# Performance work log

Hardware: AMD Instinct MI355X
Metric: run time of the kernel (lower is better)

## Reference

```python
import jax, jax.numpy as jnp
import numpy as np

NEG_INF = -9e15
NEG_SLOPE = 0.2

def setup_inputs() -> dict:
    key = jax.random.key(0)
    k1, k2, k3, k4 = jax.random.split(key, 4)
    N, d_in, d_out = 8192, 256, 256
    x = jax.random.normal(k1, (N, d_in), dtype=jnp.float32)
    adj = jax.random.randint(k2, (N, N), 0, 2).astype(jnp.float32)
    W = jax.random.normal(k3, (d_in, d_out), dtype=jnp.float32) * (1.0 / np.sqrt(d_in))
    a = jax.random.normal(k4, (2 * d_out,), dtype=jnp.float32) * (1.0 / np.sqrt(2 * d_out))
    return {"x": x, "adj": adj, "W": W, "a": a}

def reference(x, adj, W, a):
    d_out = W.shape[1]
    Wh = x @ W                                   # [N, d_out]
    # a([Wh_i || Wh_j]) decomposed: e_ij = <a_src, Wh_i> + <a_dst, Wh_j>
    e_src = Wh @ a[:d_out]                       # [N]
    e_dst = Wh @ a[d_out:]                       # [N]
    e = jax.nn.leaky_relu(e_src[:, None] + e_dst[None, :], NEG_SLOPE)  # [N, N]
    N = Wh.shape[0]
    mask = (adj > 0) | jnp.eye(N, dtype=bool)
    e = jnp.where(mask, e, NEG_INF)
    alpha = jax.nn.softmax(e, axis=1)            # [N, N]
    h = alpha @ Wh                               # [N, d_out]
    return h
```

## Files before the change

kernel.cpp:

```cpp
#include <hip/hip_runtime.h>
#include <stdint.h>

#define N 8192
#define D 256

typedef __attribute__((ext_vector_type(4))) float f32x4;
typedef __attribute__((ext_vector_type(8))) short bf16x8;

__device__ __forceinline__ unsigned short f2bf(float f) {
    unsigned u = __float_as_uint(f);
    u += 0x7fff + ((u >> 16) & 1);
    return (unsigned short)(u >> 16);
}
__device__ __forceinline__ float leaky(float x) {
    return fmaxf(x, 0.f) + 0.2f * fminf(x, 0.f);
}
__device__ __forceinline__ void sync_lds() {
    asm volatile("s_waitcnt lgkmcnt(0)\n\ts_barrier" ::: "memory");
}

__global__ __launch_bounds__(256) void k0_compress(const float* __restrict__ adj,
                                                   unsigned int* __restrict__ mask) {
    const int idx = blockIdx.x * 256 + threadIdx.x;
    const int r = idx >> 8;
    const int ww = idx & 255;
    const float* src = adj + ((size_t)idx << 5);
    unsigned int bits = 0;
#pragma unroll
    for (int j = 0; j < 8; ++j) {
        float4 v = *(const float4*)(src + j * 4);
        bits |= (v.x > 0.f ? 1u : 0u) << (j * 4 + 0);
        bits |= (v.y > 0.f ? 1u : 0u) << (j * 4 + 1);
        bits |= (v.z > 0.f ? 1u : 0u) << (j * 4 + 2);
        bits |= (v.w > 0.f ? 1u : 0u) << (j * 4 + 3);
    }
    if ((r >> 5) == ww) bits |= 1u << (r & 31);
    mask[idx] = bits;
}

#define K1_BM 16
__global__ __launch_bounds__(256) void k1_gemm(const float* __restrict__ x,
                                               const float* __restrict__ W,
                                               float* __restrict__ Wh,
                                               unsigned short* __restrict__ WhT) {
    __shared__ float xsT[32][20];
    const int t = threadIdx.x;
    const int r0 = blockIdx.x * K1_BM;
    float acc[K1_BM];
#pragma unroll
    for (int i = 0; i < K1_BM; ++i) acc[i] = 0.f;

    for (int k0 = 0; k0 < D; k0 += 32) {
        __syncthreads();
        if (t < 128) {
            int r = t >> 3, ks = (t & 7) * 4;
            float4 v = *(const float4*)(x + (size_t)(r0 + r) * D + k0 + ks);
            xsT[ks + 0][r] = v.x; xsT[ks + 1][r] = v.y;
            xsT[ks + 2][r] = v.z; xsT[ks + 3][r] = v.w;
        }
        __syncthreads();
#pragma unroll 8
        for (int kk = 0; kk < 32; ++kk) {
            float wv = W[(size_t)(k0 + kk) * D + t];
#pragma unroll
            for (int rc = 0; rc < K1_BM / 4; ++rc) {
                float4 xv = *(const float4*)&xsT[kk][rc * 4];
                acc[rc * 4 + 0] += xv.x * wv;
                acc[rc * 4 + 1] += xv.y * wv;
                acc[rc * 4 + 2] += xv.z * wv;
                acc[rc * 4 + 3] += xv.w * wv;
            }
        }
    }
#pragma unroll
    for (int r = 0; r < K1_BM; ++r) Wh[(size_t)(r0 + r) * D + t] = acc[r];
    unsigned short pk[K1_BM];
#pragma unroll
    for (int r = 0; r < K1_BM; ++r) pk[r] = f2bf(acc[r]);
    uint4* dst = (uint4*)(WhT + (size_t)t * N + r0);
    dst[0] = *(uint4*)&pk[0];
    dst[1] = *(uint4*)&pk[8];
}

__global__ __launch_bounds__(256) void k2_edot(const float* __restrict__ Wh,
                                               const float* __restrict__ a,
                                               float* __restrict__ e_src,
                                               float* __restrict__ e_dst) {
    const int wave = threadIdx.x >> 6, lane = threadIdx.x & 63;
    const int row = blockIdx.x * 4 + wave;
    float4 wv = *(const float4*)(Wh + (size_t)row * D + lane * 4);
    float4 as = *(const float4*)(a + lane * 4);
    float4 ad = *(const float4*)(a + D + lane * 4);
    float ps = wv.x * as.x + wv.y * as.y + wv.z * as.z + wv.w * as.w;
    float pd = wv.x * ad.x + wv.y * ad.y + wv.z * ad.z + wv.w * ad.w;
#pragma unroll
    for (int m = 1; m < 64; m <<= 1) {
        ps += __shfl_xor(ps, m);
        pd += __shfl_xor(pd, m);
    }
    if (lane == 0) { e_src[row] = ps; e_dst[row] = pd; }
}

__global__ __launch_bounds__(256) void k3_max(const float* __restrict__ e_dst,
                                              float* __restrict__ maxdst) {
    __shared__ float red[4];
    const int t = threadIdx.x;
    float m = -3.4e38f;
    for (int i = t; i < N; i += 256) m = fmaxf(m, e_dst[i]);
#pragma unroll
    for (int msk = 1; msk < 64; msk <<= 1) m = fmaxf(m, __shfl_xor(m, msk));
    if ((t & 63) == 0) red[t >> 6] = m;
    __syncthreads();
    if (t == 0) *maxdst = fmaxf(fmaxf(red[0], red[1]), fmaxf(red[2], red[3]));
}

#define BM 64
#define BK 64
#define RB (N / BM)
#define SPLITS 8
#define NITER ((N / SPLITS) / BK)
#define PSTRIDE 72
__global__ __launch_bounds__(512, 4) void k4_main(const unsigned char* __restrict__ mask,
                                                  const unsigned short* __restrict__ WhT,
                                                  const float* __restrict__ e_src,
                                                  const float* __restrict__ e_dst,
                                                  const float* __restrict__ maxdst,
                                                  float* __restrict__ O_part,
                                                  float* __restrict__ l_part) {
    __shared__ unsigned short p_lds[2][BM][PSTRIDE];

    const int t = threadIdx.x;
    const int rb = blockIdx.x & (RB - 1);
    const int s  = blockIdx.x >> 7;
    const int r0 = rb * BM;
    const int j0 = s * (N / SPLITS);

    const int pr = t >> 3;
    const int pcw = t & 7;
    const int pc = pcw * 8;
    const int gr = r0 + pr;

    const int w = t >> 6;
    const int lane = t & 63;
    const int quad = lane >> 4, lo = lane & 15;

    const float md = *maxdst;
    const float es = e_src[gr];
    const float m = leaky(es + md);

    f32x4 acc[4][2];
#pragma unroll
    for (int mt = 0; mt < 4; ++mt)
#pragma unroll
        for (int nt = 0; nt < 2; ++nt)
            acc[mt][nt] = (f32x4){0.f, 0.f, 0.f, 0.f};
    float lsum = 0.f;

    const unsigned char* mrow = mask + (size_t)gr * (N / 8) + (j0 >> 3) + pcw;
    const float* ed_row = e_dst + j0 + pc;
    const unsigned short* wt_base = WhT + (size_t)(w * 32 + lo) * N + j0 + quad * 8;

    unsigned int mb;
    float4 edv0, edv1;
    bf16x8 bfr[2][2];

    mb = mrow[0];
    edv0 = *(const float4*)(ed_row);
    edv1 = *(const float4*)(ed_row + 4);
#pragma unroll
    for (int ks2 = 0; ks2 < 2; ++ks2)
#pragma unroll
        for (int nt = 0; nt < 2; ++nt)
            bfr[ks2][nt] = *(const bf16x8*)(wt_base + (size_t)nt * (16 * N) + ks2 * 32);

    auto stage = [&](int buf) {
        float ev[8] = {edv0.x, edv0.y, edv0.z, edv0.w,
                       edv1.x, edv1.y, edv1.z, edv1.w};
        unsigned short pk[8];
#pragma unroll
        for (int jj = 0; jj < 8; ++jj) {
            float e = leaky(es + ev[jj]);
            float p = ((mb >> jj) & 1u) ? __expf(e - m) : 0.f;
            lsum += p;
            pk[jj] = f2bf(p);
        }
        *(uint4*)&p_lds[buf][pr][pc] = *(uint4*)pk;
    };

    stage(0);
    mb = mrow[8];
    edv0 = *(const float4*)(ed_row + BK);
    edv1 = *(const float4*)(ed_row + BK + 4);
    sync_lds();

#pragma unroll 2
    for (int it = 0; it < NITER; ++it) {
        const int cb = it & 1, nb = cb ^ 1;

#pragma unroll
        for (int ks2 = 0; ks2 < 2; ++ks2) {
            bf16x8 afr[4];
#pragma unroll
            for (int mt = 0; mt < 4; ++mt)
                afr[mt] = *(const bf16x8*)&p_lds[cb][mt * 16 + lo][ks2 * 32 + quad * 8];
#pragma unroll
            for (int nt = 0; nt < 2; ++nt)
#pragma unroll
                for (int mt = 0; mt < 4; ++mt)
                    acc[mt][nt] = __builtin_amdgcn_mfma_f32_16x16x32_bf16(
                        afr[mt], bfr[ks2][nt], acc[mt][nt], 0, 0, 0);
        }

        {
            const int itn = (it + 1 < NITER) ? it + 1 : NITER - 1;
#pragma unroll
            for (int ks2 = 0; ks2 < 2; ++ks2)
#pragma unroll
                for (int nt = 0; nt < 2; ++nt)
                    bfr[ks2][nt] = *(const bf16x8*)(wt_base + (size_t)nt * (16 * N) +
                                                    itn * BK + ks2 * 32);
        }

        if (it + 1 < NITER) {
            stage(nb);
            const int itn2 = (it + 2 < NITER) ? it + 2 : NITER - 1;
            mb = mrow[itn2 * 8];
            edv0 = *(const float4*)(ed_row + itn2 * BK);
            edv1 = *(const float4*)(ed_row + itn2 * BK + 4);
        }
        sync_lds();
    }

#pragma unroll
    for (int msk = 1; msk < 8; msk <<= 1) lsum += __shfl_xor(lsum, msk);
    if ((t & 7) == 0) l_part[(size_t)s * N + gr] = lsum;

#pragma unroll
    for (int mt = 0; mt < 4; ++mt) {
#pragma unroll
        for (int nt = 0; nt < 2; ++nt) {
            f32x4 v = acc[mt][nt];
            int col = w * 32 + nt * 16 + lo;
#pragma unroll
            for (int reg = 0; reg < 4; ++reg) {
                int row = mt * 16 + quad * 4 + reg;
                O_part[((size_t)s * N + r0 + row) * D + col] = v[reg];
            }
        }
    }
}

__global__ __launch_bounds__(256) void k5_reduce(const float* __restrict__ O_part,
                                                 const float* __restrict__ l_part,
                                                 float* __restrict__ out) {
    const int idx = blockIdx.x * 256 + threadIdx.x;
    const int r = idx >> 6;
    float lsum = 0.f;
#pragma unroll
    for (int s = 0; s < SPLITS; ++s) lsum += l_part[(size_t)s * N + r];
    f32x4 o = (f32x4){0.f, 0.f, 0.f, 0.f};
#pragma unroll
    for (int s = 0; s < SPLITS; ++s)
        o += *(const f32x4*)(O_part + (size_t)s * N * D + (size_t)idx * 4);
    const float inv = 1.f / lsum;
    *(f32x4*)(out + (size_t)idx * 4) = o * inv;
}

extern "C" void kernel_launch(void* const* d_in, const int* in_sizes, int n_in,
                              void* d_out, int out_size, void* d_ws, size_t ws_size,
                              hipStream_t stream) {
    const float* x   = (const float*)d_in[0];
    const float* adj = (const float*)d_in[1];
    const float* W   = (const float*)d_in[2];
    const float* a   = (const float*)d_in[3];
    float* out = (float*)d_out;

    char* ws = (char*)d_ws;
    float* Wh            = (float*)(ws);
    unsigned short* WhT  = (unsigned short*)(ws + 8388608);
    float* e_src         = (float*)(ws + 12582912);
    float* e_dst         = (float*)(ws + 12615680);
    float* maxdst        = (float*)(ws + 12648448);
    float* l_part        = (float*)(ws + 12648704);
    unsigned int* mask   = (unsigned int*)(ws + 13631488);
    float* O_part        = (float*)(ws + 25165824);

    k0_compress<<<N * N / 32 / 256, 256, 0, stream>>>(adj, mask);
    k1_gemm<<<N / K1_BM, 256, 0, stream>>>(x, W, Wh, WhT);
    k2_edot<<<N / 4, 256, 0, stream>>>(Wh, a, e_src, e_dst);
    k3_max<<<1, 256, 0, stream>>>(e_dst, maxdst);
    k4_main<<<RB * SPLITS, 512, 0, stream>>>((const unsigned char*)mask, WhT, e_src, e_dst,
                                             maxdst, O_part, l_part);
    k5_reduce<<<N * D / 4 / 256, 256, 0, stream>>>(O_part, l_part, out);
}
```

Measured before the change: 501.9 us.

## Coalesce adjacency compression, halve GEMM row tile, stage output through LDS

```diff
diff --git a/kernel.cpp b/kernel.cpp
--- a/kernel.cpp
+++ b/kernel.cpp
@@ -21,29 +21,30 @@
 
 __global__ __launch_bounds__(256) void k0_compress(const float* __restrict__ adj,
                                                    unsigned int* __restrict__ mask) {
-    const int idx = blockIdx.x * 256 + threadIdx.x;
-    const int r = idx >> 8;
-    const int ww = idx & 255;
-    const float* src = adj + ((size_t)idx << 5);
-    unsigned int bits = 0;
-#pragma unroll
-    for (int j = 0; j < 8; ++j) {
-        float4 v = *(const float4*)(src + j * 4);
-        bits |= (v.x > 0.f ? 1u : 0u) << (j * 4 + 0);
-        bits |= (v.y > 0.f ? 1u : 0u) << (j * 4 + 1);
-        bits |= (v.z > 0.f ? 1u : 0u) << (j * 4 + 2);
-        bits |= (v.w > 0.f ? 1u : 0u) << (j * 4 + 3);
-    }
-    if ((r >> 5) == ww) bits |= 1u << (r & 31);
-    mask[idx] = bits;
-}
-
-#define K1_BM 16
+    const size_t fbase = ((size_t)blockIdx.x * 256 + threadIdx.x) * 4;
+    float4 v = *(const float4*)(adj + fbase);
+    const int lane = threadIdx.x & 63;
+    unsigned nib = (v.x > 0.f ? 1u : 0u) | (v.y > 0.f ? 2u : 0u) |
+                   (v.z > 0.f ? 4u : 0u) | (v.w > 0.f ? 8u : 0u);
+    unsigned word = nib << ((lane & 7) * 4);
+    word |= __shfl_xor(word, 1);
+    word |= __shfl_xor(word, 2);
+    word |= __shfl_xor(word, 4);
+    if ((lane & 7) == 0) {
+        size_t widx = fbase >> 5;
+        int r = (int)(widx >> 8);
+        int ww = (int)(widx & 255);
+        if ((r >> 5) == ww) word |= 1u << (r & 31);
+        mask[widx] = word;
+    }
+}
+
+#define K1_BM 8
 __global__ __launch_bounds__(256) void k1_gemm(const float* __restrict__ x,
                                                const float* __restrict__ W,
                                                float* __restrict__ Wh,
                                                unsigned short* __restrict__ WhT) {
-    __shared__ float xsT[32][20];
+    __shared__ float xsT[32][12];
     const int t = threadIdx.x;
     const int r0 = blockIdx.x * K1_BM;
     float acc[K1_BM];
@@ -52,7 +53,7 @@
 
     for (int k0 = 0; k0 < D; k0 += 32) {
         __syncthreads();
-        if (t < 128) {
+        if (t < 64) {
             int r = t >> 3, ks = (t & 7) * 4;
             float4 v = *(const float4*)(x + (size_t)(r0 + r) * D + k0 + ks);
             xsT[ks + 0][r] = v.x; xsT[ks + 1][r] = v.y;
@@ -79,7 +80,6 @@
     for (int r = 0; r < K1_BM; ++r) pk[r] = f2bf(acc[r]);
     uint4* dst = (uint4*)(WhT + (size_t)t * N + r0);
     dst[0] = *(uint4*)&pk[0];
-    dst[1] = *(uint4*)&pk[8];
 }
 
 __global__ __launch_bounds__(256) void k2_edot(const float* __restrict__ Wh,
@@ -235,18 +235,26 @@
     for (int msk = 1; msk < 8; msk <<= 1) lsum += __shfl_xor(lsum, msk);
     if ((t & 7) == 0) l_part[(size_t)s * N + gr] = lsum;
 
+    float* obuf = (float*)p_lds;
 #pragma unroll
     for (int mt = 0; mt < 4; ++mt) {
+        __syncthreads();
 #pragma unroll
         for (int nt = 0; nt < 2; ++nt) {
             f32x4 v = acc[mt][nt];
             int col = w * 32 + nt * 16 + lo;
 #pragma unroll
-            for (int reg = 0; reg < 4; ++reg) {
-                int row = mt * 16 + quad * 4 + reg;
-                O_part[((size_t)s * N + r0 + row) * D + col] = v[reg];
-            }
-        }
+            for (int reg = 0; reg < 4; ++reg)
+                obuf[(quad * 4 + reg) * 256 + col] = v[reg];
+        }
+        __syncthreads();
+        const int orow = t >> 5;
+        const int ocol = (t & 31) * 8;
+        f32x4 o0 = *(const f32x4*)&obuf[orow * 256 + ocol];
+        f32x4 o1 = *(const f32x4*)&obuf[orow * 256 + ocol + 4];
+        float* dst = O_part + ((size_t)s * N + r0 + mt * 16 + orow) * D + ocol;
+        *(f32x4*)dst = o0;
+        *(f32x4*)(dst + 4) = o1;
     }
 }
 
@@ -285,7 +293,7 @@
     unsigned int* mask   = (unsigned int*)(ws + 13631488);
     float* O_part        = (float*)(ws + 25165824);
 
-    k0_compress<<<N * N / 32 / 256, 256, 0, stream>>>(adj, mask);
+    k0_compress<<<N * N / 4 / 256, 256, 0, stream>>>(adj, mask);
     k1_gemm<<<N / K1_BM, 256, 0, stream>>>(x, W, Wh, WhT);
     k2_edot<<<N / 4, 256, 0, stream>>>(Wh, a, e_src, e_dst);
     k3_max<<<1, 256, 0, stream>>>(e_dst, maxdst);
```

After: 484.7 us. 3.4% less time.
